# Kernel tuning notes

Measured on AMD Instinct MI355X. Metric: run time of the kernel, lower is better.

The kernel has to match this reference:

```python
import jax, jax.numpy as jnp
import numpy as np

D_MODEL = 1024
D_KEY = 64
BATCH = 4
SEQ = 4096


def setup_inputs() -> dict:
    key = jax.random.key(0)
    kq, kk, kv, kwq, kwk, kwv = jax.random.split(key, 6)
    queries = jax.random.normal(kq, (BATCH, SEQ, D_MODEL), dtype=jnp.float32)
    keys = jax.random.normal(kk, (BATCH, SEQ, D_MODEL), dtype=jnp.float32)
    values = jax.random.normal(kv, (BATCH, SEQ, D_MODEL), dtype=jnp.float32)
    # causal mask: 1 = keep, 0 = masked out (torch masked_fill where mask==0)
    mask = jnp.tril(jnp.ones((SEQ, SEQ), dtype=jnp.int32))
    s = 1.0 / np.sqrt(D_MODEL)
    Wq = jax.random.normal(kwq, (D_MODEL, D_KEY), dtype=jnp.float32) * s
    Wk = jax.random.normal(kwk, (D_MODEL, D_KEY), dtype=jnp.float32) * s
    Wv = jax.random.normal(kwv, (D_MODEL, D_KEY), dtype=jnp.float32) * s
    return {"queries": queries, "keys": keys, "values": values,
            "mask": mask, "Wq": Wq, "Wk": Wk, "Wv": Wv}


def reference(queries, keys, values, mask, Wq, Wk, Wv):
    q = jnp.einsum('bsd,dk->bsk', queries, Wq)   # [B,S,dk]
    k = jnp.einsum('bsd,dk->bsk', keys, Wk)
    v = jnp.einsum('bsd,dk->bsk', values, Wv)
    scale = 1.0 / np.sqrt(D_KEY).astype(np.float32)
    attn = jnp.einsum('bqk,bsk->bqs', q, k) * scale  # [B,Sq,Sk]
    attn = jnp.where(mask == 0, -jnp.inf, attn)
    attn = jax.nn.softmax(attn, axis=-1)
    return jnp.einsum('bqs,bsk->bqk', attn, v)      # [B,S,dk]
```

## Files before the change

### kernel.cpp

```cpp
#include <hip/hip_runtime.h>
#include <hip/hip_bf16.h>

#define B      4
#define SEQ    4096
#define DM     1024
#define DK     64
#define NSPLIT 4

typedef __bf16 bf16x8 __attribute__((ext_vector_type(8)));
typedef __bf16 bf16x4 __attribute__((ext_vector_type(4)));
typedef float  f32x4  __attribute__((ext_vector_type(4)));

#define KSTR 72

__global__ __launch_bounds__(256) void wt_kernel(
    const float* __restrict__ Wq, const float* __restrict__ Wk,
    const float* __restrict__ Wv, __bf16* __restrict__ Wt)
{
    const int mat = blockIdx.y;
    const float* W = (mat == 0) ? Wq : (mat == 1) ? Wk : Wv;
    const int k0 = blockIdx.x * 64;
    const int tid = threadIdx.x;

    __shared__ float t[64][65];

    const int r = tid >> 2;
    const int c = (tid & 3) * 16;
    {
        const float* src = W + (size_t)(k0 + r) * DK + c;
        #pragma unroll
        for (int j = 0; j < 4; ++j) {
            float4 a = *(const float4*)(src + j * 4);
            t[r][c + j * 4 + 0] = a.x; t[r][c + j * 4 + 1] = a.y;
            t[r][c + j * 4 + 2] = a.z; t[r][c + j * 4 + 3] = a.w;
        }
    }
    __syncthreads();
    const int n  = tid >> 2;
    const int kk = (tid & 3) * 16;
    bf16x8 b0, b1;
    #pragma unroll
    for (int j = 0; j < 8; ++j) b0[j] = (__bf16)t[kk + j][n];
    #pragma unroll
    for (int j = 0; j < 8; ++j) b1[j] = (__bf16)t[kk + 8 + j][n];
    __bf16* dst = Wt + (size_t)(mat * DK + n) * DM + k0 + kk;
    *(bf16x8*)(dst)     = b0;
    *(bf16x8*)(dst + 8) = b1;
}

__global__ __launch_bounds__(256) void proj_stream_kernel(
    const float* __restrict__ q_in, const float* __restrict__ k_in,
    const float* __restrict__ v_in, const __bf16* __restrict__ Wt,
    __bf16* __restrict__ qb, __bf16* __restrict__ kb,
    __bf16* __restrict__ vtb)
{
    const int m = blockIdx.y;
    const float* in = (m == 0) ? q_in : (m == 1) ? k_in : v_in;
    const __bf16* wt = Wt + (size_t)m * DK * DM;

    const int rowbase = blockIdx.x * 64;
    const int tid  = threadIdx.x;
    const int w    = tid >> 6;
    const int lane = tid & 63;
    const int quad = lane >> 4;
    const int l15  = lane & 15;

    const float*  arow = in + (size_t)(rowbase + w * 16 + l15) * DM;
    const __bf16* wrow = wt + (size_t)l15 * DM + quad * 8;

    f32x4 acc[4];
    #pragma unroll
    for (int nf = 0; nf < 4; ++nf) acc[nf] = (f32x4){0.f, 0.f, 0.f, 0.f};

    float4 a0 = *(const float4*)(arow + quad * 8);
    float4 a1 = *(const float4*)(arow + quad * 8 + 4);
    bf16x8 w0 = *(const bf16x8*)(wrow);
    bf16x8 w1 = *(const bf16x8*)(wrow + 16 * DM);
    bf16x8 w2 = *(const bf16x8*)(wrow + 32 * DM);
    bf16x8 w3 = *(const bf16x8*)(wrow + 48 * DM);

    #pragma unroll 4
    for (int kc = 0; kc < DM; kc += 32) {
        float4 b0, b1; bf16x8 x0, x1, x2, x3;
        const int kn = kc + 32;
        if (kn < DM) {
            const float* ap = arow + kn + quad * 8;
            b0 = *(const float4*)(ap);
            b1 = *(const float4*)(ap + 4);
            const __bf16* wp = wrow + kn;
            x0 = *(const bf16x8*)(wp);
            x1 = *(const bf16x8*)(wp + 16 * DM);
            x2 = *(const bf16x8*)(wp + 32 * DM);
            x3 = *(const bf16x8*)(wp + 48 * DM);
        }
        bf16x8 af;
        af[0] = (__bf16)a0.x; af[1] = (__bf16)a0.y;
        af[2] = (__bf16)a0.z; af[3] = (__bf16)a0.w;
        af[4] = (__bf16)a1.x; af[5] = (__bf16)a1.y;
        af[6] = (__bf16)a1.z; af[7] = (__bf16)a1.w;
        acc[0] = __builtin_amdgcn_mfma_f32_16x16x32_bf16(af, w0, acc[0], 0, 0, 0);
        acc[1] = __builtin_amdgcn_mfma_f32_16x16x32_bf16(af, w1, acc[1], 0, 0, 0);
        acc[2] = __builtin_amdgcn_mfma_f32_16x16x32_bf16(af, w2, acc[2], 0, 0, 0);
        acc[3] = __builtin_amdgcn_mfma_f32_16x16x32_bf16(af, w3, acc[3], 0, 0, 0);
        a0 = b0; a1 = b1; w0 = x0; w1 = x1; w2 = x2; w3 = x3;
    }

    if (m < 2) {
        __bf16* outb = (m == 0) ? qb : kb;
        #pragma unroll
        for (int nf = 0; nf < 4; ++nf)
            #pragma unroll
            for (int r = 0; r < 4; ++r)
                outb[(size_t)(rowbase + w * 16 + quad * 4 + r) * DK + nf * 16 + l15] =
                    (__bf16)acc[nf][r];
    } else {
        const int bb = rowbase >> 12;
        const int s0 = (rowbase & (SEQ - 1)) + w * 16 + quad * 4;
        #pragma unroll
        for (int nf = 0; nf < 4; ++nf) {
            bf16x4 v4;
            #pragma unroll
            for (int r = 0; r < 4; ++r) v4[r] = (__bf16)acc[nf][r];
            *(bf16x4*)&vtb[(size_t)(bb * DK + nf * 16 + l15) * SEQ + s0] = v4;
        }
    }
}

__global__ __launch_bounds__(256) void flash_kernel(
    const __bf16* __restrict__ qb, const __bf16* __restrict__ kb,
    const __bf16* __restrict__ vtb, float* __restrict__ Opart,
    float* __restrict__ lpart)
{
    const int qt  = blockIdx.x;
    const int bb  = blockIdx.y;
    const int z   = blockIdx.z;
    const int tid = threadIdx.x;
    const int w    = tid >> 6;
    const int lane = tid & 63;
    const int quad = lane >> 4;
    const int l15  = lane & 15;

    __shared__ __bf16 Ks[64 * KSTR];
    __shared__ __bf16 Vs[64 * KSTR];
    __shared__ __bf16 Ps[4][16 * KSTR];

    const int qrow_base = qt * 64 + w * 16;
    const int niters = qt + 1;
    const int kt0 = (niters * z) / NSPLIT;
    const int kt1 = (niters * (z + 1)) / NSPLIT;

    bf16x8 qf[2];
    {
        const __bf16* qp = qb + ((size_t)(bb * SEQ + qrow_base + l15)) * DK + quad * 8;
        qf[0] = *(const bf16x8*)(qp);
        qf[1] = *(const bf16x8*)(qp + 32);
    }

    bf16x8 ones;
    #pragma unroll
    for (int j = 0; j < 8; ++j) ones[j] = (__bf16)1.0f;

    f32x4 of[4], lacc;
    #pragma unroll
    for (int nf = 0; nf < 4; ++nf) of[nf] = (f32x4){0.f, 0.f, 0.f, 0.f};
    lacc = (f32x4){0.f, 0.f, 0.f, 0.f};

    const float SC = 0.125f * 1.44269504088896340736f;
    const float M2 = 12.0f;

    for (int kt = kt0; kt < kt1; ++kt) {
        __syncthreads();
        {
            const int r  = tid >> 2;
            const int cc = (tid & 3) * 16;
            const __bf16* kg = kb + ((size_t)(bb * SEQ + kt * 64 + r)) * DK + cc;
            *(bf16x8*)(&Ks[r * KSTR + cc])     = *(const bf16x8*)(kg);
            *(bf16x8*)(&Ks[r * KSTR + cc + 8]) = *(const bf16x8*)(kg + 8);
            const __bf16* vg = vtb + ((size_t)(bb * DK + r)) * SEQ + kt * 64 + cc;
            *(bf16x8*)(&Vs[r * KSTR + cc])     = *(const bf16x8*)(vg);
            *(bf16x8*)(&Vs[r * KSTR + cc + 8]) = *(const bf16x8*)(vg + 8);
        }
        __syncthreads();

        f32x4 sf[4];
        #pragma unroll
        for (int nf = 0; nf < 4; ++nf) {
            sf[nf] = (f32x4){0.f, 0.f, 0.f, 0.f};
            #pragma unroll
            for (int ch = 0; ch < 2; ++ch) {
                bf16x8 kf = *(const bf16x8*)(&Ks[(nf * 16 + l15) * KSTR + ch * 32 + quad * 8]);
                sf[nf] = __builtin_amdgcn_mfma_f32_16x16x32_bf16(qf[ch], kf, sf[nf], 0, 0, 0);
            }
        }

        const bool diag = (kt == qt);
        #pragma unroll
        for (int nf = 0; nf < 4; ++nf) {
            #pragma unroll
            for (int r = 0; r < 4; ++r) {
                float s = sf[nf][r] * SC;
                if (diag) {
                    const int kcol = nf * 16 + l15;
                    const int qrow = w * 16 + quad * 4 + r;
                    if (kcol > qrow) s = -1.0e9f;
                }
                const float p = __builtin_amdgcn_exp2f(s - M2);
                Ps[w][(quad * 4 + r) * KSTR + nf * 16 + l15] = (__bf16)p;
            }
        }

        bf16x8 pf[2];
        pf[0] = *(const bf16x8*)(&Ps[w][l15 * KSTR + quad * 8]);
        pf[1] = *(const bf16x8*)(&Ps[w][l15 * KSTR + 32 + quad * 8]);
        lacc = __builtin_amdgcn_mfma_f32_16x16x32_bf16(pf[0], ones, lacc, 0, 0, 0);
        lacc = __builtin_amdgcn_mfma_f32_16x16x32_bf16(pf[1], ones, lacc, 0, 0, 0);
        #pragma unroll
        for (int nf = 0; nf < 4; ++nf) {
            #pragma unroll
            for (int ch = 0; ch < 2; ++ch) {
                bf16x8 vf = *(const bf16x8*)(&Vs[(nf * 16 + l15) * KSTR + ch * 32 + quad * 8]);
                of[nf] = __builtin_amdgcn_mfma_f32_16x16x32_bf16(pf[ch], vf, of[nf], 0, 0, 0);
            }
        }
    }

    float* Op = Opart + ((size_t)(z * B + bb) * SEQ + qrow_base) * DK;
    #pragma unroll
    for (int nf = 0; nf < 4; ++nf)
        #pragma unroll
        for (int r = 0; r < 4; ++r)
            Op[(size_t)(quad * 4 + r) * DK + nf * 16 + l15] = of[nf][r];
    if (l15 == 0) {
        const size_t base = (size_t)(z * B + bb) * SEQ + qrow_base + quad * 4;
        #pragma unroll
        for (int r = 0; r < 4; ++r)
            lpart[base + r] = lacc[r];
    }
}

__global__ __launch_bounds__(256) void combine_kernel(
    const float* __restrict__ Opart, const float* __restrict__ lpart,
    float* __restrict__ out)
{
    const int idx = blockIdx.x * 256 + threadIdx.x;
    const int col = idx & (DK - 1);
    const int row = idx >> 6;

    float L = 0.f, o = 0.f;
    #pragma unroll
    for (int z = 0; z < NSPLIT; ++z) {
        L += lpart[(size_t)z * (B * SEQ) + row];
        o += Opart[((size_t)z * (B * SEQ) + row) * DK + col];
    }
    out[idx] = o / L;
}

extern "C" void kernel_launch(void* const* d_in, const int* in_sizes, int n_in,
                              void* d_out, int out_size, void* d_ws, size_t ws_size,
                              hipStream_t stream)
{
    const float* queries = (const float*)d_in[0];
    const float* keys    = (const float*)d_in[1];
    const float* values  = (const float*)d_in[2];
    const float* Wq = (const float*)d_in[4];
    const float* Wk = (const float*)d_in[5];
    const float* Wv = (const float*)d_in[6];
    float* out = (float*)d_out;

    char* p = (char*)d_ws;
    __bf16* qb  = (__bf16*)p;  p += (size_t)B * SEQ * DK * 2;
    __bf16* kb  = (__bf16*)p;  p += (size_t)B * SEQ * DK * 2;
    __bf16* vtb = (__bf16*)p;  p += (size_t)B * SEQ * DK * 2;
    __bf16* Wt  = (__bf16*)p;  p += (size_t)3 * DK * DM * 2;
    float* Opart = (float*)p;  p += (size_t)NSPLIT * B * SEQ * DK * 4;
    float* lpart = (float*)p;  p += (size_t)NSPLIT * B * SEQ * 4;

    wt_kernel<<<dim3(DM / 64, 3), 256, 0, stream>>>(Wq, Wk, Wv, Wt);

    proj_stream_kernel<<<dim3((B * SEQ) / 64, 3), 256, 0, stream>>>(
        queries, keys, values, Wt, qb, kb, vtb);

    flash_kernel<<<dim3(SEQ / 64, B, NSPLIT), 256, 0, stream>>>(
        qb, kb, vtb, Opart, lpart);

    combine_kernel<<<(B * SEQ * DK) / 256, 256, 0, stream>>>(
        Opart, lpart, out);
}
```

Before: 302.1 us.

## Widen flash query tiles, prefetch K/V, deepen projection loads, fold scale into Wq

The flash kernel now handles 128 query rows per block, two 16-row groups per wave, so each K/V tile loaded into LDS is reused twice. It also prefetches the next K/V tile into registers while the current one is computed. The split count rises to 8, and the partial outputs are stored as bf16 to cut combine traffic. The softmax scale is folded into Wq and the bias into the accumulator initial value. The projection kernel gets a deeper register prefetch ring. The changes add register pressure and lower the precision of the partial outputs.

After: 290.8 us. -3.7%, faster.

```diff
diff --git a/kernel.cpp b/kernel.cpp
--- a/kernel.cpp
+++ b/kernel.cpp
@@ -5,7 +5,7 @@
 #define SEQ    4096
 #define DM     1024
 #define DK     64
-#define NSPLIT 4
+#define NSPLIT 8
 
 typedef __bf16 bf16x8 __attribute__((ext_vector_type(8)));
 typedef __bf16 bf16x4 __attribute__((ext_vector_type(4)));
@@ -13,12 +13,16 @@
 
 #define KSTR 72
 
+#define QSCALE 0.1803368801111204f
+#define M2BIAS 12.0f
+
 __global__ __launch_bounds__(256) void wt_kernel(
     const float* __restrict__ Wq, const float* __restrict__ Wk,
     const float* __restrict__ Wv, __bf16* __restrict__ Wt)
 {
     const int mat = blockIdx.y;
     const float* W = (mat == 0) ? Wq : (mat == 1) ? Wk : Wv;
+    const float scale = (mat == 0) ? QSCALE : 1.0f;
     const int k0 = blockIdx.x * 64;
     const int tid = threadIdx.x;
 
@@ -40,14 +44,16 @@
     const int kk = (tid & 3) * 16;
     bf16x8 b0, b1;
     #pragma unroll
-    for (int j = 0; j < 8; ++j) b0[j] = (__bf16)t[kk + j][n];
-    #pragma unroll
-    for (int j = 0; j < 8; ++j) b1[j] = (__bf16)t[kk + 8 + j][n];
+    for (int j = 0; j < 8; ++j) b0[j] = (__bf16)(t[kk + j][n] * scale);
+    #pragma unroll
+    for (int j = 0; j < 8; ++j) b1[j] = (__bf16)(t[kk + 8 + j][n] * scale);
     __bf16* dst = Wt + (size_t)(mat * DK + n) * DM + k0 + kk;
     *(bf16x8*)(dst)     = b0;
     *(bf16x8*)(dst + 8) = b1;
 }
 
+#define DA 8
+#define DW 4
 __global__ __launch_bounds__(256) void proj_stream_kernel(
     const float* __restrict__ q_in, const float* __restrict__ k_in,
     const float* __restrict__ v_in, const __bf16* __restrict__ Wt,
@@ -65,44 +71,55 @@
     const int quad = lane >> 4;
     const int l15  = lane & 15;
 
-    const float*  arow = in + (size_t)(rowbase + w * 16 + l15) * DM;
+    const float*  arow = in + (size_t)(rowbase + w * 16 + l15) * DM + quad * 8;
     const __bf16* wrow = wt + (size_t)l15 * DM + quad * 8;
 
+    float4 Aa[DA], Ab[DA];
+    bf16x8 Wb[DW][4];
+    #pragma unroll
+    for (int d = 0; d < DA; ++d) {
+        const float* ap = arow + d * 32;
+        Aa[d] = *(const float4*)(ap);
+        Ab[d] = *(const float4*)(ap + 4);
+    }
+    #pragma unroll
+    for (int d = 0; d < DW; ++d) {
+        const __bf16* wp = wrow + d * 32;
+        Wb[d][0] = *(const bf16x8*)(wp);
+        Wb[d][1] = *(const bf16x8*)(wp + 16 * DM);
+        Wb[d][2] = *(const bf16x8*)(wp + 32 * DM);
+        Wb[d][3] = *(const bf16x8*)(wp + 48 * DM);
+    }
+
     f32x4 acc[4];
     #pragma unroll
     for (int nf = 0; nf < 4; ++nf) acc[nf] = (f32x4){0.f, 0.f, 0.f, 0.f};
 
-    float4 a0 = *(const float4*)(arow + quad * 8);
-    float4 a1 = *(const float4*)(arow + quad * 8 + 4);
-    bf16x8 w0 = *(const bf16x8*)(wrow);
-    bf16x8 w1 = *(const bf16x8*)(wrow + 16 * DM);
-    bf16x8 w2 = *(const bf16x8*)(wrow + 32 * DM);
-    bf16x8 w3 = *(const bf16x8*)(wrow + 48 * DM);
-
-    #pragma unroll 4
-    for (int kc = 0; kc < DM; kc += 32) {
-        float4 b0, b1; bf16x8 x0, x1, x2, x3;
-        const int kn = kc + 32;
-        if (kn < DM) {
-            const float* ap = arow + kn + quad * 8;
-            b0 = *(const float4*)(ap);
-            b1 = *(const float4*)(ap + 4);
-            const __bf16* wp = wrow + kn;
-            x0 = *(const bf16x8*)(wp);
-            x1 = *(const bf16x8*)(wp + 16 * DM);
-            x2 = *(const bf16x8*)(wp + 32 * DM);
-            x3 = *(const bf16x8*)(wp + 48 * DM);
-        }
+    #pragma unroll
+    for (int it = 0; it < 32; ++it) {
+        const int da = it & (DA - 1);
+        const int dw = it & (DW - 1);
         bf16x8 af;
-        af[0] = (__bf16)a0.x; af[1] = (__bf16)a0.y;
-        af[2] = (__bf16)a0.z; af[3] = (__bf16)a0.w;
-        af[4] = (__bf16)a1.x; af[5] = (__bf16)a1.y;
-        af[6] = (__bf16)a1.z; af[7] = (__bf16)a1.w;
-        acc[0] = __builtin_amdgcn_mfma_f32_16x16x32_bf16(af, w0, acc[0], 0, 0, 0);
-        acc[1] = __builtin_amdgcn_mfma_f32_16x16x32_bf16(af, w1, acc[1], 0, 0, 0);
-        acc[2] = __builtin_amdgcn_mfma_f32_16x16x32_bf16(af, w2, acc[2], 0, 0, 0);
-        acc[3] = __builtin_amdgcn_mfma_f32_16x16x32_bf16(af, w3, acc[3], 0, 0, 0);
-        a0 = b0; a1 = b1; w0 = x0; w1 = x1; w2 = x2; w3 = x3;
+        af[0] = (__bf16)Aa[da].x; af[1] = (__bf16)Aa[da].y;
+        af[2] = (__bf16)Aa[da].z; af[3] = (__bf16)Aa[da].w;
+        af[4] = (__bf16)Ab[da].x; af[5] = (__bf16)Ab[da].y;
+        af[6] = (__bf16)Ab[da].z; af[7] = (__bf16)Ab[da].w;
+        acc[0] = __builtin_amdgcn_mfma_f32_16x16x32_bf16(af, Wb[dw][0], acc[0], 0, 0, 0);
+        acc[1] = __builtin_amdgcn_mfma_f32_16x16x32_bf16(af, Wb[dw][1], acc[1], 0, 0, 0);
+        acc[2] = __builtin_amdgcn_mfma_f32_16x16x32_bf16(af, Wb[dw][2], acc[2], 0, 0, 0);
+        acc[3] = __builtin_amdgcn_mfma_f32_16x16x32_bf16(af, Wb[dw][3], acc[3], 0, 0, 0);
+        if (it + DA < 32) {
+            const float* ap = arow + (it + DA) * 32;
+            Aa[da] = *(const float4*)(ap);
+            Ab[da] = *(const float4*)(ap + 4);
+        }
+        if (it + DW < 32) {
+            const __bf16* wp = wrow + (it + DW) * 32;
+            Wb[dw][0] = *(const bf16x8*)(wp);
+            Wb[dw][1] = *(const bf16x8*)(wp + 16 * DM);
+            Wb[dw][2] = *(const bf16x8*)(wp + 32 * DM);
+            Wb[dw][3] = *(const bf16x8*)(wp + 48 * DM);
+        }
     }
 
     if (m < 2) {
@@ -128,7 +145,7 @@
 
 __global__ __launch_bounds__(256) void flash_kernel(
     const __bf16* __restrict__ qb, const __bf16* __restrict__ kb,
-    const __bf16* __restrict__ vtb, float* __restrict__ Opart,
+    const __bf16* __restrict__ vtb, __bf16* __restrict__ Opart,
     float* __restrict__ lpart)
 {
     const int qt  = blockIdx.x;
@@ -142,115 +159,146 @@
 
     __shared__ __bf16 Ks[64 * KSTR];
     __shared__ __bf16 Vs[64 * KSTR];
-    __shared__ __bf16 Ps[4][16 * KSTR];
-
-    const int qrow_base = qt * 64 + w * 16;
-    const int niters = qt + 1;
+    __shared__ __bf16 Ps[4][2][16 * KSTR];
+
+    const int qrow_base = qt * 128 + w * 32;
+    const int niters = 2 * qt + 2;
     const int kt0 = (niters * z) / NSPLIT;
     const int kt1 = (niters * (z + 1)) / NSPLIT;
 
-    bf16x8 qf[2];
-    {
-        const __bf16* qp = qb + ((size_t)(bb * SEQ + qrow_base + l15)) * DK + quad * 8;
-        qf[0] = *(const bf16x8*)(qp);
-        qf[1] = *(const bf16x8*)(qp + 32);
+    bf16x8 qf[2][2];
+    #pragma unroll
+    for (int g = 0; g < 2; ++g) {
+        const __bf16* qp = qb + ((size_t)(bb * SEQ + qrow_base + g * 16 + l15)) * DK + quad * 8;
+        qf[g][0] = *(const bf16x8*)(qp);
+        qf[g][1] = *(const bf16x8*)(qp + 32);
     }
 
     bf16x8 ones;
     #pragma unroll
     for (int j = 0; j < 8; ++j) ones[j] = (__bf16)1.0f;
 
-    f32x4 of[4], lacc;
-    #pragma unroll
-    for (int nf = 0; nf < 4; ++nf) of[nf] = (f32x4){0.f, 0.f, 0.f, 0.f};
-    lacc = (f32x4){0.f, 0.f, 0.f, 0.f};
-
-    const float SC = 0.125f * 1.44269504088896340736f;
-    const float M2 = 12.0f;
+    f32x4 of[2][4], lacc[2];
+    #pragma unroll
+    for (int g = 0; g < 2; ++g) {
+        #pragma unroll
+        for (int nf = 0; nf < 4; ++nf) of[g][nf] = (f32x4){0.f, 0.f, 0.f, 0.f};
+        lacc[g] = (f32x4){0.f, 0.f, 0.f, 0.f};
+    }
+
+    const int sr = tid >> 2;
+    const int sc = (tid & 3) * 16;
+    bf16x8 kr0, kr1, vr0, vr1;
+    const __bf16* kbase = kb  + ((size_t)(bb * SEQ + sr)) * DK + sc;
+    const __bf16* vbase = vtb + ((size_t)(bb * DK  + sr)) * SEQ + sc;
+
+    if (kt1 > kt0) {
+        const __bf16* kg = kbase + (size_t)kt0 * 64 * DK;
+        kr0 = *(const bf16x8*)(kg); kr1 = *(const bf16x8*)(kg + 8);
+        const __bf16* vg = vbase + kt0 * 64;
+        vr0 = *(const bf16x8*)(vg); vr1 = *(const bf16x8*)(vg + 8);
+    }
 
     for (int kt = kt0; kt < kt1; ++kt) {
         __syncthreads();
-        {
-            const int r  = tid >> 2;
-            const int cc = (tid & 3) * 16;
-            const __bf16* kg = kb + ((size_t)(bb * SEQ + kt * 64 + r)) * DK + cc;
-            *(bf16x8*)(&Ks[r * KSTR + cc])     = *(const bf16x8*)(kg);
-            *(bf16x8*)(&Ks[r * KSTR + cc + 8]) = *(const bf16x8*)(kg + 8);
-            const __bf16* vg = vtb + ((size_t)(bb * DK + r)) * SEQ + kt * 64 + cc;
-            *(bf16x8*)(&Vs[r * KSTR + cc])     = *(const bf16x8*)(vg);
-            *(bf16x8*)(&Vs[r * KSTR + cc + 8]) = *(const bf16x8*)(vg + 8);
-        }
+        *(bf16x8*)&Ks[sr * KSTR + sc]     = kr0;
+        *(bf16x8*)&Ks[sr * KSTR + sc + 8] = kr1;
+        *(bf16x8*)&Vs[sr * KSTR + sc]     = vr0;
+        *(bf16x8*)&Vs[sr * KSTR + sc + 8] = vr1;
         __syncthreads();
-
-        f32x4 sf[4];
+        if (kt + 1 < kt1) {
+            const __bf16* kg = kbase + (size_t)(kt + 1) * 64 * DK;
+            kr0 = *(const bf16x8*)(kg); kr1 = *(const bf16x8*)(kg + 8);
+            const __bf16* vg = vbase + (kt + 1) * 64;
+            vr0 = *(const bf16x8*)(vg); vr1 = *(const bf16x8*)(vg + 8);
+        }
+
+        f32x4 sf[2][4];
+        #pragma unroll
+        for (int g = 0; g < 2; ++g)
+            #pragma unroll
+            for (int nf = 0; nf < 4; ++nf)
+                sf[g][nf] = (f32x4){-M2BIAS, -M2BIAS, -M2BIAS, -M2BIAS};
         #pragma unroll
         for (int nf = 0; nf < 4; ++nf) {
-            sf[nf] = (f32x4){0.f, 0.f, 0.f, 0.f};
             #pragma unroll
             for (int ch = 0; ch < 2; ++ch) {
                 bf16x8 kf = *(const bf16x8*)(&Ks[(nf * 16 + l15) * KSTR + ch * 32 + quad * 8]);
-                sf[nf] = __builtin_amdgcn_mfma_f32_16x16x32_bf16(qf[ch], kf, sf[nf], 0, 0, 0);
+                sf[0][nf] = __builtin_amdgcn_mfma_f32_16x16x32_bf16(qf[0][ch], kf, sf[0][nf], 0, 0, 0);
+                sf[1][nf] = __builtin_amdgcn_mfma_f32_16x16x32_bf16(qf[1][ch], kf, sf[1][nf], 0, 0, 0);
             }
         }
 
-        const bool diag = (kt == qt);
-        #pragma unroll
-        for (int nf = 0; nf < 4; ++nf) {
-            #pragma unroll
-            for (int r = 0; r < 4; ++r) {
-                float s = sf[nf][r] * SC;
-                if (diag) {
-                    const int kcol = nf * 16 + l15;
-                    const int qrow = w * 16 + quad * 4 + r;
-                    if (kcol > qrow) s = -1.0e9f;
+        const int kc0 = kt * 64;
+        #pragma unroll
+        for (int g = 0; g < 2; ++g) {
+            const int r0 = qrow_base + g * 16;
+            const bool dg = (kc0 + 63 > r0);
+            #pragma unroll
+            for (int nf = 0; nf < 4; ++nf) {
+                #pragma unroll
+                for (int r = 0; r < 4; ++r) {
+                    float s = sf[g][nf][r];
+                    if (dg) {
+                        const int col = kc0 + nf * 16 + l15;
+                        const int row = r0 + quad * 4 + r;
+                        if (col > row) s = -1.0e9f;
+                    }
+                    const float p = __builtin_amdgcn_exp2f(s);
+                    Ps[w][g][(quad * 4 + r) * KSTR + nf * 16 + l15] = (__bf16)p;
                 }
-                const float p = __builtin_amdgcn_exp2f(s - M2);
-                Ps[w][(quad * 4 + r) * KSTR + nf * 16 + l15] = (__bf16)p;
             }
         }
 
-        bf16x8 pf[2];
-        pf[0] = *(const bf16x8*)(&Ps[w][l15 * KSTR + quad * 8]);
-        pf[1] = *(const bf16x8*)(&Ps[w][l15 * KSTR + 32 + quad * 8]);
-        lacc = __builtin_amdgcn_mfma_f32_16x16x32_bf16(pf[0], ones, lacc, 0, 0, 0);
-        lacc = __builtin_amdgcn_mfma_f32_16x16x32_bf16(pf[1], ones, lacc, 0, 0, 0);
+        bf16x8 pf[2][2];
+        #pragma unroll
+        for (int g = 0; g < 2; ++g) {
+            pf[g][0] = *(const bf16x8*)(&Ps[w][g][l15 * KSTR + quad * 8]);
+            pf[g][1] = *(const bf16x8*)(&Ps[w][g][l15 * KSTR + 32 + quad * 8]);
+            lacc[g] = __builtin_amdgcn_mfma_f32_16x16x32_bf16(pf[g][0], ones, lacc[g], 0, 0, 0);
+            lacc[g] = __builtin_amdgcn_mfma_f32_16x16x32_bf16(pf[g][1], ones, lacc[g], 0, 0, 0);
+        }
+
         #pragma unroll
         for (int nf = 0; nf < 4; ++nf) {
             #pragma unroll
             for (int ch = 0; ch < 2; ++ch) {
                 bf16x8 vf = *(const bf16x8*)(&Vs[(nf * 16 + l15) * KSTR + ch * 32 + quad * 8]);
-                of[nf] = __builtin_amdgcn_mfma_f32_16x16x32_bf16(pf[ch], vf, of[nf], 0, 0, 0);
+                of[0][nf] = __builtin_amdgcn_mfma_f32_16x16x32_bf16(pf[0][ch], vf, of[0][nf], 0, 0, 0);
+                of[1][nf] = __builtin_amdgcn_mfma_f32_16x16x32_bf16(pf[1][ch], vf, of[1][nf], 0, 0, 0);
             }
         }
     }
 
-    float* Op = Opart + ((size_t)(z * B + bb) * SEQ + qrow_base) * DK;
-    #pragma unroll
-    for (int nf = 0; nf < 4; ++nf)
-        #pragma unroll
-        for (int r = 0; r < 4; ++r)
-            Op[(size_t)(quad * 4 + r) * DK + nf * 16 + l15] = of[nf][r];
-    if (l15 == 0) {
-        const size_t base = (size_t)(z * B + bb) * SEQ + qrow_base + quad * 4;
-        #pragma unroll
-        for (int r = 0; r < 4; ++r)
-            lpart[base + r] = lacc[r];
+    #pragma unroll
+    for (int g = 0; g < 2; ++g) {
+        __bf16* Op = Opart + ((size_t)(z * B + bb) * SEQ + qrow_base + g * 16) * DK;
+        #pragma unroll
+        for (int nf = 0; nf < 4; ++nf)
+            #pragma unroll
+            for (int r = 0; r < 4; ++r)
+                Op[(size_t)(quad * 4 + r) * DK + nf * 16 + l15] = (__bf16)of[g][nf][r];
+        if (l15 == 0) {
+            const size_t base = (size_t)(z * B + bb) * SEQ + qrow_base + g * 16 + quad * 4;
+            #pragma unroll
+            for (int r = 0; r < 4; ++r)
+                lpart[base + r] = lacc[g][r];
+        }
     }
 }
 
 __global__ __launch_bounds__(256) void combine_kernel(
-    const float* __restrict__ Opart, const float* __restrict__ lpart,
+    const __bf16* __restrict__ Opart, const float* __restrict__ lpart,
     float* __restrict__ out)
 {
     const int idx = blockIdx.x * 256 + threadIdx.x;
-    const int col = idx & (DK - 1);
     const int row = idx >> 6;
 
     float L = 0.f, o = 0.f;
     #pragma unroll
     for (int z = 0; z < NSPLIT; ++z) {
         L += lpart[(size_t)z * (B * SEQ) + row];
-        o += Opart[((size_t)z * (B * SEQ) + row) * DK + col];
+        o += (float)Opart[(size_t)z * (B * SEQ) * DK + idx];
     }
     out[idx] = o / L;
 }
@@ -272,15 +320,15 @@
     __bf16* kb  = (__bf16*)p;  p += (size_t)B * SEQ * DK * 2;
     __bf16* vtb = (__bf16*)p;  p += (size_t)B * SEQ * DK * 2;
     __bf16* Wt  = (__bf16*)p;  p += (size_t)3 * DK * DM * 2;
-    float* Opart = (float*)p;  p += (size_t)NSPLIT * B * SEQ * DK * 4;
-    float* lpart = (float*)p;  p += (size_t)NSPLIT * B * SEQ * 4;
+    __bf16* Opart = (__bf16*)p; p += (size_t)NSPLIT * B * SEQ * DK * 2;
+    float* lpart = (float*)p;   p += (size_t)NSPLIT * B * SEQ * 4;
 
     wt_kernel<<<dim3(DM / 64, 3), 256, 0, stream>>>(Wq, Wk, Wv, Wt);
 
     proj_stream_kernel<<<dim3((B * SEQ) / 64, 3), 256, 0, stream>>>(
         queries, keys, values, Wt, qb, kb, vtb);
 
-    flash_kernel<<<dim3(SEQ / 64, B, NSPLIT), 256, 0, stream>>>(
+    flash_kernel<<<dim3(SEQ / 128, B, NSPLIT), 256, 0, stream>>>(
         qb, kb, vtb, Opart, lpart);
 
     combine_kernel<<<(B * SEQ * DK) / 256, 256, 0, stream>>>(
```
